# Optimization experiments

Measured on AMD Instinct MI355X. Metric: run time of the kernel, lower is better.

The kernel has to match this reference:

```python
import jax, jax.numpy as jnp
import numpy as np

N, E, G = 100_000, 1_200_000, 256
EPS = 1e-5

def _bn(a, g, b):
    # BatchNorm1d in training mode: biased batch statistics over dim 0
    mu = a.mean(0)
    var = ((a - mu) ** 2).mean(0)
    return (a - mu) * jax.lax.rsqrt(var + EPS) * g + b

def _cgconv(x, src, dst, ea, Wf, bf, Ws, bs, g, b):
    # PyG CGConv: z = [x_i, x_j, edge_attr]; m = sigmoid(lin_f(z)) * softplus(lin_s(z));
    # out = BN(scatter_add(m -> dst)) + x
    z = jnp.concatenate([x[dst], x[src], ea], axis=-1)      # [E, 2*64+1]
    m = jax.nn.sigmoid(z @ Wf + bf) * jax.nn.softplus(z @ Ws + bs)  # [E, 64]
    agg = jax.ops.segment_sum(m, dst, num_segments=x.shape[0])
    return _bn(agg, g, b) + x

def setup_inputs() -> dict:
    key = jax.random.key(0)
    ks = jax.random.split(key, 16)
    def w(k, shape, scale):
        return jax.random.normal(k, shape, jnp.float32) * scale
    inp = {
        "x": jax.random.normal(ks[0], (N, 12), jnp.float32),
        "edge_index": jax.random.randint(ks[1], (2, E), 0, N, jnp.int32),
        "edge_attr": jax.random.uniform(ks[2], (E, 1), dtype=jnp.float32),
        "batch": jnp.sort(jax.random.randint(ks[3], (N,), 0, G, jnp.int32)),
        "W_in": w(ks[4], (12, 64), 0.3), "b_in": jnp.zeros((64,), jnp.float32),
        "g0": jnp.ones((64,), jnp.float32), "beta0": jnp.zeros((64,), jnp.float32),
    }
    i = 5
    for l in (1, 2, 3):
        inp[f"Wf{l}"] = w(ks[i], (129, 64), 0.1)
        inp[f"bf{l}"] = jnp.zeros((64,), jnp.float32)
        inp[f"Ws{l}"] = w(ks[i + 1], (129, 64), 0.1)
        inp[f"bs{l}"] = jnp.zeros((64,), jnp.float32)
        inp[f"g{l}"] = jnp.ones((64,), jnp.float32)
        inp[f"bb{l}"] = jnp.zeros((64,), jnp.float32)
        i += 2
    inp["W1"] = w(ks[11], (64, 32), 0.15)
    inp["b1"] = jnp.zeros((32,), jnp.float32)
    inp["W2"] = w(ks[12], (32, 1), 0.2)
    inp["b2"] = jnp.zeros((1,), jnp.float32)
    return inp

def reference(x, edge_index, edge_attr, batch,
              W_in, b_in, g0, beta0,
              Wf1, bf1, Ws1, bs1, g1, bb1,
              Wf2, bf2, Ws2, bs2, g2, bb2,
              Wf3, bf3, Ws3, bs3, g3, bb3,
              W1, b1, W2, b2):
    src, dst = edge_index[0], edge_index[1]
    h = jax.nn.relu(_bn(x @ W_in + b_in, g0, beta0))
    h = jax.nn.relu(_cgconv(h, src, dst, edge_attr, Wf1, bf1, Ws1, bs1, g1, bb1))
    h = jax.nn.relu(_cgconv(h, src, dst, edge_attr, Wf2, bf2, Ws2, bs2, g2, bb2))
    h = _cgconv(h, src, dst, edge_attr, Wf3, bf3, Ws3, bs3, g3, bb3)
    # global_mean_pool
    s = jax.ops.segment_sum(h, batch, num_segments=G)
    c = jax.ops.segment_sum(jnp.ones((h.shape[0],), h.dtype), batch, num_segments=G)
    pooled = s / jnp.maximum(c, 1.0)[:, None]
    return jax.nn.relu(pooled @ W1 + b1) @ W2 + b2  # [G, 1]
```

## Files before the change

### kernel.cpp

```cpp
#include <hip/hip_runtime.h>
#include <math.h>

#define N_NODES 100000
#define N_EDGES 1200000
#define N_GRAPHS 256
#define CH 64
#define NC (N_NODES * CH)
#define EPS 1e-5f
#define LOG2E 1.4426950408889634f
#define LN2 0.6931471805599453f
#define EA_SCALE 32768.0f

#define SCAN_NB 98
#define ZSTRN 72
#define GTILES ((N_NODES + 63) / 64)
#define EA_BLOCKS 4096
#define NW (EA_BLOCKS * 4)
#define POOL_BLOCKS 256
#define WP2ROWS 64

#define NCOLORS 8
#define SC_BLOCKS 2048
#define NCHUNK (SC_BLOCKS / NCOLORS)
#define CSZ ((N_EDGES + NCHUNK - 1) / NCHUNK)
#define RNODES ((N_NODES + NCOLORS - 1) / NCOLORS)

typedef _Float16 half8 __attribute__((ext_vector_type(8)));
typedef _Float16 half2v __attribute__((ext_vector_type(2)));
typedef float floatx4 __attribute__((ext_vector_type(4)));

__device__ __forceinline__ int lbound(const int* __restrict__ a, int n, int v) {
    int lo = 0, hi = n;
    while (lo < hi) {
        int mid = (lo + hi) >> 1;
        if (a[mid] < v) lo = mid + 1; else hi = mid;
    }
    return lo;
}

__device__ __forceinline__ float gate2(float f2, float s2) {
    float ef = __builtin_amdgcn_exp2f(-f2);
    float sig = __builtin_amdgcn_rcpf(1.0f + ef);
    float es = __builtin_amdgcn_exp2f(-fabsf(s2));
    float sp = fmaxf(s2, 0.0f) + __builtin_amdgcn_logf(1.0f + es);
    return sig * sp;
}

__global__ void embed_stats_kernel(const float* __restrict__ x,
                                   const float* __restrict__ W,
                                   const float* __restrict__ b,
                                   float* __restrict__ out,
                                   float* __restrict__ stats) {
    int c = threadIdx.x & 63;
    int sub = threadIdx.x >> 6;
    float s = 0.f, q = 0.f;
    for (int r = blockIdx.x * 4 + sub; r < N_NODES; r += gridDim.x * 4) {
        const float* xr = x + r * 12;
        float acc = b[c];
#pragma unroll
        for (int k = 0; k < 12; ++k)
            acc = fmaf(xr[k], W[k * CH + c], acc);
        out[(size_t)r * CH + c] = acc;
        s += acc;
        q = fmaf(acc, acc, q);
    }
    __shared__ float ls[4][64];
    __shared__ float lq[4][64];
    ls[sub][c] = s;
    lq[sub][c] = q;
    __syncthreads();
    if (sub == 0) {
        s = ls[0][c] + ls[1][c] + ls[2][c] + ls[3][c];
        q = lq[0][c] + lq[1][c] + lq[2][c] + lq[3][c];
        atomicAdd(&stats[c], s);
        atomicAdd(&stats[64 + c], q);
    }
}

__global__ void hist_kernel(const int* __restrict__ ei,
                            int* __restrict__ rowptr) {
    const int j = blockIdx.x & (NCOLORS - 1);
    const int k = blockIdx.x >> 3;
    const int dlo = j * RNODES;
    const int dhi = min(N_NODES, dlo + RNODES);
    const int e0 = k * CSZ;
    const int e1 = min(N_EDGES, e0 + CSZ);
    for (int e = e0 + threadIdx.x; e < e1; e += 256) {
        int d = ei[N_EDGES + e];
        if (d >= dlo && d < dhi) atomicAdd(&rowptr[d + 1], 1);
    }
}

__global__ void scanA_kernel(int* __restrict__ a, int* __restrict__ btot) {
    __shared__ int wsum[16];
    int t = threadIdx.x, lane = t & 63, w = t >> 6;
    int i = blockIdx.x * 1024 + t;
    int v = (i <= N_NODES) ? a[i] : 0;
    int s = v;
#pragma unroll
    for (int d = 1; d < 64; d <<= 1) {
        int o = __shfl_up(s, d);
        if (lane >= d) s += o;
    }
    if (lane == 63) wsum[w] = s;
    __syncthreads();
    if (w == 0) {
        int ws2 = (lane < 16) ? wsum[lane] : 0;
#pragma unroll
        for (int d = 1; d < 16; d <<= 1) {
            int o = __shfl_up(ws2, d);
            if (lane >= d) ws2 += o;
        }
        if (lane < 16) wsum[lane] = ws2;
    }
    __syncthreads();
    int off = (w > 0) ? wsum[w - 1] : 0;
    if (i <= N_NODES) a[i] = s + off;
    if (t == 0) btot[blockIdx.x] = wsum[15];
}

__global__ void scanB_kernel(int* __restrict__ btot) {
    int lane = threadIdx.x;
    int carry = 0;
    for (int base = 0; base < SCAN_NB; base += 64) {
        int i = base + lane;
        int v = (i < SCAN_NB) ? btot[i] : 0;
        int s = v;
#pragma unroll
        for (int d = 1; d < 64; d <<= 1) {
            int o = __shfl_up(s, d);
            if (lane >= d) s += o;
        }
        if (i < SCAN_NB) btot[i] = s + carry;
        carry += __shfl(s, 63);
    }
}

__global__ void scanC_kernel(int* __restrict__ a, const int* __restrict__ btot,
                             int* __restrict__ cursor) {
    int i = blockIdx.x * 1024 + threadIdx.x;
    int off = (blockIdx.x > 0) ? btot[blockIdx.x - 1] : 0;
    if (i <= N_NODES) {
        int val = a[i] + off;
        a[i] = val;
        if (i < N_NODES) cursor[i] = val;
    }
}

__global__ void scatter_kernel(const int* __restrict__ ei,
                               const float* __restrict__ ea,
                               int* __restrict__ cursor,
                               unsigned* __restrict__ sef,
                               const int* __restrict__ rowptr,
                               int* __restrict__ wrange) {
    int gid = blockIdx.x * blockDim.x + threadIdx.x;
    if (gid <= NW) {
        if (gid == NW) wrange[NW] = N_NODES;
        else {
            int e0t = (int)((long)gid * N_EDGES / NW);
            wrange[gid] = lbound(rowptr, N_NODES + 1, e0t);
        }
    }
    if (gid < 8) sef[N_EDGES + gid] = 0u;
    const int j = blockIdx.x & (NCOLORS - 1);
    const int k = blockIdx.x >> 3;
    const int dlo = j * RNODES;
    const int dhi = min(N_NODES, dlo + RNODES);
    const int e0 = k * CSZ;
    const int e1 = min(N_EDGES, e0 + CSZ);
    for (int e = e0 + threadIdx.x; e < e1; e += 256) {
        int d = ei[N_EDGES + e];
        if (d >= dlo && d < dhi) {
            int pos = atomicAdd(&cursor[d], 1);
            unsigned v = ((unsigned)ei[e] << 15) | (unsigned)(ea[e] * EA_SCALE);
            sef[pos] = v;
        }
    }
}

__global__ void prep_weights_kernel(const float* __restrict__ Wf0, const float* __restrict__ Ws0,
                                    const float* __restrict__ bf0, const float* __restrict__ bs0,
                                    const float* __restrict__ Wf1, const float* __restrict__ Ws1,
                                    const float* __restrict__ bf1, const float* __restrict__ bs1,
                                    const float* __restrict__ Wf2, const float* __restrict__ Ws2,
                                    const float* __restrict__ bf2, const float* __restrict__ bs2,
                                    _Float16* __restrict__ WT2,
                                    float* __restrict__ w128,
                                    float* __restrict__ bias) {
    int gid = blockIdx.x * blockDim.x + threadIdx.x;
    int l = gid >> 14;
    int idx = gid & 16383;
    if (l >= 3) return;
    const float* Wf = (l == 0) ? Wf0 : (l == 1) ? Wf1 : Wf2;
    const float* Ws = (l == 0) ? Ws0 : (l == 1) ? Ws1 : Ws2;
    const float* bf = (l == 0) ? bf0 : (l == 1) ? bf1 : bf2;
    const float* bs = (l == 0) ? bs0 : (l == 1) ? bs1 : bs2;
    {
        int cc = idx >> 6;
        int k = idx & 63;
        float v;
        if (cc < 128) {
            int ch = cc >> 1;
            v = (cc & 1) ? Ws[k * 64 + ch] : Wf[k * 64 + ch];
        } else {
            int j = cc - 128, ch = j >> 1;
            v = (j & 1) ? Ws[(64 + k) * 64 + ch] : Wf[(64 + k) * 64 + ch];
        }
        WT2[l * 16384 + idx] = (_Float16)(v * LOG2E);
    }
    if (idx < 128) {
        w128[l * 128 + idx] = ((idx < 64) ? Wf[128 * 64 + idx] : Ws[128 * 64 + (idx - 64)])
                              * (LOG2E / EA_SCALE);
        bias[l * 128 + idx] = ((idx < 64) ? bf[idx] : bs[idx - 64]) * LOG2E;
    }
}

template <bool RES, bool RED, bool A16>
__global__ __launch_bounds__(256)
void node_gemm_kernel(const void* __restrict__ ain,
                      const float* __restrict__ res,
                      const float* __restrict__ stats,
                      const float* __restrict__ gamma,
                      const float* __restrict__ beta,
                      const _Float16* __restrict__ WT2,
                      float* __restrict__ hout,
                      _Float16* __restrict__ pqrs) {
    __shared__ __align__(16) _Float16 As[64 * ZSTRN];
    __shared__ __align__(16) float ab[128];
    __shared__ float sw[128];
    const int t = threadIdx.x;
    const int lane = t & 63;
    const int w = t >> 6;
    const int l15 = lane & 15;
    const int quad = lane >> 4;

    if (RED) {
        if (t < 128) {
            float s = 0.f;
#pragma unroll 8
            for (int r = 0; r < WP2ROWS; ++r) s += stats[r * 128 + t];
            sw[t] = s;
        }
        __syncthreads();
    }
    if (t < 64) {
        float s0 = RED ? sw[t] : stats[t];
        float s1 = RED ? sw[64 + t] : stats[64 + t];
        float mean = s0 * (1.0f / (float)N_NODES);
        float var  = s1 * (1.0f / (float)N_NODES) - mean * mean;
        float inv  = rsqrtf(var + EPS);
        float A = gamma[t] * inv;
        ab[t] = A;
        ab[64 + t] = beta[t] - mean * A;
    }

    half8 bfr[4][2];
#pragma unroll
    for (int tt = 0; tt < 4; ++tt)
#pragma unroll
        for (int ks = 0; ks < 2; ++ks)
            bfr[tt][ks] = *(const half8*)(WT2 + (w * 64 + tt * 16 + l15) * 64 + ks * 32 + quad * 8);
    __syncthreads();

    const int base = blockIdx.x * 64;
    {
        const int e = t >> 2, q = t & 3;
        const int row = base + e;
        const bool valid = (row < N_NODES);
        const int crow = valid ? row : (N_NODES - 1);
        const float* rp = res + (size_t)crow * CH + q * 16;
        float af[16];
        if (A16) {
            const _Float16* aph = (const _Float16*)ain + (size_t)crow * CH + q * 16;
            half8 h0 = *(const half8*)aph;
            half8 h1 = *(const half8*)(aph + 8);
#pragma unroll
            for (int j = 0; j < 8; ++j) { af[j] = (float)h0[j]; af[8 + j] = (float)h1[j]; }
        } else {
            const float* ap = (const float*)ain + (size_t)crow * CH + q * 16;
#pragma unroll
            for (int i = 0; i < 4; ++i) {
                float4 a4 = *(const float4*)(ap + i * 4);
                af[i * 4 + 0] = a4.x; af[i * 4 + 1] = a4.y;
                af[i * 4 + 2] = a4.z; af[i * 4 + 3] = a4.w;
            }
        }
        float vv[16];
#pragma unroll
        for (int i = 0; i < 4; ++i) {
            float4 A4 = *(const float4*)(ab + q * 16 + i * 4);
            float4 B4 = *(const float4*)(ab + 64 + q * 16 + i * 4);
            float rx = 0.f, ry = 0.f, rz = 0.f, rw = 0.f;
            if (RES) {
                float4 r4 = *(const float4*)(rp + i * 4);
                rx = r4.x; ry = r4.y; rz = r4.z; rw = r4.w;
            }
            vv[i * 4 + 0] = fmaxf(fmaf(af[i * 4 + 0], A4.x, B4.x) + rx, 0.0f);
            vv[i * 4 + 1] = fmaxf(fmaf(af[i * 4 + 1], A4.y, B4.y) + ry, 0.0f);
            vv[i * 4 + 2] = fmaxf(fmaf(af[i * 4 + 2], A4.z, B4.z) + rz, 0.0f);
            vv[i * 4 + 3] = fmaxf(fmaf(af[i * 4 + 3], A4.w, B4.w) + rw, 0.0f);
        }
        if (valid) {
            float* hp = hout + (size_t)row * CH + q * 16;
#pragma unroll
            for (int i = 0; i < 4; ++i)
                *(float4*)(hp + i * 4) = make_float4(vv[i * 4], vv[i * 4 + 1], vv[i * 4 + 2], vv[i * 4 + 3]);
        }
        half8 o;
#pragma unroll
        for (int j = 0; j < 8; ++j) o[j] = (_Float16)vv[j];
        *(half8*)(As + e * ZSTRN + q * 16) = o;
#pragma unroll
        for (int j = 0; j < 8; ++j) o[j] = (_Float16)vv[8 + j];
        *(half8*)(As + e * ZSTRN + q * 16 + 8) = o;
    }
    __syncthreads();

    floatx4 acc[4][4];
#pragma unroll
    for (int rt = 0; rt < 4; ++rt)
#pragma unroll
        for (int tt = 0; tt < 4; ++tt)
#pragma unroll
            for (int r = 0; r < 4; ++r) acc[rt][tt][r] = 0.f;

#pragma unroll
    for (int ks = 0; ks < 2; ++ks) {
#pragma unroll
        for (int rt = 0; rt < 4; ++rt) {
            half8 a = *(const half8*)(As + (rt * 16 + l15) * ZSTRN + ks * 32 + quad * 8);
#pragma unroll
            for (int tt = 0; tt < 4; ++tt)
                acc[rt][tt] = __builtin_amdgcn_mfma_f32_16x16x32_f16(a, bfr[tt][ks], acc[rt][tt], 0, 0, 0);
        }
    }

#pragma unroll
    for (int rt = 0; rt < 4; ++rt) {
#pragma unroll
        for (int r = 0; r < 4; ++r) {
            int row = base + rt * 16 + quad * 4 + r;
            if (row < N_NODES) {
#pragma unroll
                for (int tt = 0; tt < 4; ++tt)
                    pqrs[(size_t)row * 256 + w * 64 + tt * 16 + l15] = (_Float16)acc[rt][tt][r];
            }
        }
    }
}

__global__ __launch_bounds__(256)
void edge_agg_kernel(const _Float16* __restrict__ pqrs,
                     const unsigned* __restrict__ sef,
                     const int* __restrict__ rowptr,
                     const int* __restrict__ wrange,
                     const float* __restrict__ w128,
                     const float* __restrict__ bias,
                     _Float16* __restrict__ agg,
                     float* __restrict__ wpart2) {
    const int lane = threadIdx.x & 63;
    const int w = threadIdx.x >> 6;
    const int gw = __builtin_amdgcn_readfirstlane(blockIdx.x * 4 + w);
    const float wfc = w128[lane], wsc = w128[64 + lane];
    const float bfc = bias[lane], bsc = bias[64 + lane];
    const half2v* __restrict__ prb = (const half2v*)pqrs;
    const half2v* __restrict__ qsb = (const half2v*)pqrs + 64;

    const int n0 = wrange[gw];
    const int n1 = wrange[gw + 1];

    float ssum = 0.f, sqsum = 0.f;
    for (int n = n0; n < n1; ++n) {
        const int rs = rowptr[n], re = rowptr[n + 1];
        half2v pr = prb[(size_t)n * 128 + lane];
        const float fb = (float)pr[0] + bfc;
        const float sb = (float)pr[1] + bsc;
        float acc0 = 0.f, acc1 = 0.f, acc2 = 0.f, acc3 = 0.f;
        int e = rs;
        for (; e + 8 <= re; e += 8) {
            unsigned s0 = sef[e],     s1 = sef[e + 1], s2 = sef[e + 2], s3 = sef[e + 3];
            unsigned s4 = sef[e + 4], s5 = sef[e + 5], s6 = sef[e + 6], s7 = sef[e + 7];
            half2v q0 = qsb[(size_t)(s0 >> 15) * 128 + lane];
            half2v q1 = qsb[(size_t)(s1 >> 15) * 128 + lane];
            half2v q2 = qsb[(size_t)(s2 >> 15) * 128 + lane];
            half2v q3 = qsb[(size_t)(s3 >> 15) * 128 + lane];
            half2v q4 = qsb[(size_t)(s4 >> 15) * 128 + lane];
            half2v q5 = qsb[(size_t)(s5 >> 15) * 128 + lane];
            half2v q6 = qsb[(size_t)(s6 >> 15) * 128 + lane];
            half2v q7 = qsb[(size_t)(s7 >> 15) * 128 + lane];
            float ea0 = (float)(s0 & 32767u), ea1 = (float)(s1 & 32767u);
            float ea2 = (float)(s2 & 32767u), ea3 = (float)(s3 & 32767u);
            float ea4 = (float)(s4 & 32767u), ea5 = (float)(s5 & 32767u);
            float ea6 = (float)(s6 & 32767u), ea7 = (float)(s7 & 32767u);
            acc0 += gate2(fmaf(ea0, wfc, fb + (float)q0[0]), fmaf(ea0, wsc, sb + (float)q0[1]));
            acc1 += gate2(fmaf(ea1, wfc, fb + (float)q1[0]), fmaf(ea1, wsc, sb + (float)q1[1]));
            acc2 += gate2(fmaf(ea2, wfc, fb + (float)q2[0]), fmaf(ea2, wsc, sb + (float)q2[1]));
            acc3 += gate2(fmaf(ea3, wfc, fb + (float)q3[0]), fmaf(ea3, wsc, sb + (float)q3[1]));
            acc0 += gate2(fmaf(ea4, wfc, fb + (float)q4[0]), fmaf(ea4, wsc, sb + (float)q4[1]));
            acc1 += gate2(fmaf(ea5, wfc, fb + (float)q5[0]), fmaf(ea5, wsc, sb + (float)q5[1]));
            acc2 += gate2(fmaf(ea6, wfc, fb + (float)q6[0]), fmaf(ea6, wsc, sb + (float)q6[1]));
            acc3 += gate2(fmaf(ea7, wfc, fb + (float)q7[0]), fmaf(ea7, wsc, sb + (float)q7[1]));
        }
        if (e + 4 <= re) {
            unsigned s0 = sef[e], s1 = sef[e + 1], s2 = sef[e + 2], s3 = sef[e + 3];
            half2v q0 = qsb[(size_t)(s0 >> 15) * 128 + lane];
            half2v q1 = qsb[(size_t)(s1 >> 15) * 128 + lane];
            half2v q2 = qsb[(size_t)(s2 >> 15) * 128 + lane];
            half2v q3 = qsb[(size_t)(s3 >> 15) * 128 + lane];
            float ea0 = (float)(s0 & 32767u), ea1 = (float)(s1 & 32767u);
            float ea2 = (float)(s2 & 32767u), ea3 = (float)(s3 & 32767u);
            acc0 += gate2(fmaf(ea0, wfc, fb + (float)q0[0]), fmaf(ea0, wsc, sb + (float)q0[1]));
            acc1 += gate2(fmaf(ea1, wfc, fb + (float)q1[0]), fmaf(ea1, wsc, sb + (float)q1[1]));
            acc2 += gate2(fmaf(ea2, wfc, fb + (float)q2[0]), fmaf(ea2, wsc, sb + (float)q2[1]));
            acc3 += gate2(fmaf(ea3, wfc, fb + (float)q3[0]), fmaf(ea3, wsc, sb + (float)q3[1]));
            e += 4;
        }
        for (; e < re; ++e) {
            unsigned s0 = sef[e];
            half2v q0 = qsb[(size_t)(s0 >> 15) * 128 + lane];
            float ea0 = (float)(s0 & 32767u);
            acc0 += gate2(fmaf(ea0, wfc, fb + (float)q0[0]), fmaf(ea0, wsc, sb + (float)q0[1]));
        }
        _Float16 ah = (_Float16)(LN2 * ((acc0 + acc1) + (acc2 + acc3)));
        agg[(size_t)n * CH + lane] = ah;
        float acc = (float)ah;
        ssum += acc;
        sqsum = fmaf(acc, acc, sqsum);
    }
    __shared__ float reds[4][128];
    reds[w][lane] = ssum;
    reds[w][64 + lane] = sqsum;
    __syncthreads();
    if (w == 0) {
        float a = reds[0][lane] + reds[1][lane] + reds[2][lane] + reds[3][lane];
        float b = reds[0][64 + lane] + reds[1][64 + lane] + reds[2][64 + lane] + reds[3][64 + lane];
        float* wp = wpart2 + (size_t)(blockIdx.x & (WP2ROWS - 1)) * 128;
        atomicAdd(&wp[lane], a);
        atomicAdd(&wp[64 + lane], b);
    }
}

__global__ __launch_bounds__(256)
void pool_bn_kernel(const _Float16* __restrict__ ain,
                    const float* __restrict__ res,
                    const float* __restrict__ wp2,
                    const float* __restrict__ gamma,
                    const float* __restrict__ beta,
                    const int* __restrict__ batch,
                    float* __restrict__ pooled,
                    float* __restrict__ counts) {
    __shared__ float sw[128];
    __shared__ float ab[128];
    if (threadIdx.x < 128) {
        float s = 0.f;
#pragma unroll 8
        for (int r = 0; r < WP2ROWS; ++r) s += wp2[r * 128 + threadIdx.x];
        sw[threadIdx.x] = s;
    }
    __syncthreads();
    if (threadIdx.x < 64) {
        int t = threadIdx.x;
        float mean = sw[t] * (1.0f / (float)N_NODES);
        float var  = sw[64 + t] * (1.0f / (float)N_NODES) - mean * mean;
        float inv  = rsqrtf(var + EPS);
        float A = gamma[t] * inv;
        ab[t] = A;
        ab[64 + t] = beta[t] - mean * A;
    }
    __syncthreads();

    const int c = threadIdx.x & 63;
    const float A = ab[c], B = ab[64 + c];
    const int walker = blockIdx.x * 4 + (threadIdx.x >> 6);
    const int nwalk = POOL_BLOCKS * 4;
    const int chunk = (N_NODES + nwalk - 1) / nwalk;
    int r0 = walker * chunk;
    int r1 = min(N_NODES, r0 + chunk);
    if (r0 >= r1) return;

    int cur = batch[r0];
    float acc = 0.0f;
    int runlen = 0;
    for (int r = r0; r < r1; ++r) {
        int b = batch[r];
        if (b != cur) {
            atomicAdd(&pooled[cur * CH + c], acc);
            if (c == 0) atomicAdd(&counts[cur], (float)runlen);
            acc = 0.0f;
            runlen = 0;
            cur = b;
        }
        size_t idx = (size_t)r * CH + c;
        acc += fmaf((float)ain[idx], A, B) + res[idx];
        ++runlen;
    }
    atomicAdd(&pooled[cur * CH + c], acc);
    if (c == 0) atomicAdd(&counts[cur], (float)runlen);
}

__global__ void head_kernel(const float* __restrict__ pooled,
                            const float* __restrict__ counts,
                            const float* __restrict__ W1,
                            const float* __restrict__ b1,
                            const float* __restrict__ W2,
                            const float* __restrict__ b2,
                            float* __restrict__ out) {
    int gph = blockIdx.x;
    int t = threadIdx.x;
    __shared__ float p[64];
    __shared__ float h1[32];
    float cnt = fmaxf(counts[gph], 1.0f);
    p[t] = pooled[gph * CH + t] / cnt;
    __syncthreads();
    if (t < 32) {
        float acc = b1[t];
#pragma unroll
        for (int c = 0; c < 64; ++c)
            acc = fmaf(p[c], W1[c * 32 + t], acc);
        h1[t] = fmaxf(acc, 0.0f);
    }
    __syncthreads();
    if (t == 0) {
        float acc = b2[0];
#pragma unroll
        for (int j = 0; j < 32; ++j)
            acc = fmaf(h1[j], W2[j], acc);
        out[gph] = acc;
    }
}

extern "C" void kernel_launch(void* const* d_in, const int* in_sizes, int n_in,
                              void* d_out, int out_size, void* d_ws, size_t ws_size,
                              hipStream_t stream) {
    const float* x     = (const float*)d_in[0];
    const int*   ei    = (const int*)d_in[1];
    const float* ea    = (const float*)d_in[2];
    const int*   batch = (const int*)d_in[3];
    const float* W_in  = (const float*)d_in[4];
    const float* b_in  = (const float*)d_in[5];
    const float* g0    = (const float*)d_in[6];
    const float* beta0 = (const float*)d_in[7];

    const float* Wf[3] = {(const float*)d_in[8],  (const float*)d_in[14], (const float*)d_in[20]};
    const float* bfv[3]= {(const float*)d_in[9],  (const float*)d_in[15], (const float*)d_in[21]};
    const float* Wsv[3]= {(const float*)d_in[10], (const float*)d_in[16], (const float*)d_in[22]};
    const float* bsv[3]= {(const float*)d_in[11], (const float*)d_in[17], (const float*)d_in[23]};
    const float* gm[3] = {(const float*)d_in[12], (const float*)d_in[18], (const float*)d_in[24]};
    const float* bb[3] = {(const float*)d_in[13], (const float*)d_in[19], (const float*)d_in[25]};

    const float* W1 = (const float*)d_in[26];
    const float* b1 = (const float*)d_in[27];
    const float* W2 = (const float*)d_in[28];
    const float* b2 = (const float*)d_in[29];

    float* out = (float*)d_out;

#define ALIGN256(v) (((v) + 255) & ~(size_t)255)
    char* base = (char*)d_ws;
    size_t off = 0;
    float* bufA = (float*)(base + off);       off = ALIGN256(off + (size_t)NC * 4);
    float* bufB = (float*)(base + off);       off = ALIGN256(off + (size_t)NC * 4);
    _Float16* AGG = (_Float16*)(base + off);  off = ALIGN256(off + (size_t)NC * 2);
    _Float16* WT2 = (_Float16*)(base + off);  off = ALIGN256(off + 3 * 256 * 64 * 2);
    float* w128   = (float*)(base + off);     off = ALIGN256(off + 3 * 128 * 4);
    float* biasL  = (float*)(base + off);     off = ALIGN256(off + 3 * 128 * 4);
    int* cursor   = (int*)(base + off);       off = ALIGN256(off + (size_t)N_NODES * 4);
    unsigned* sef = (unsigned*)(base + off);  off = ALIGN256(off + (size_t)(N_EDGES + 8) * 4);
    _Float16* pqrs = (_Float16*)(base + off); off = ALIGN256(off + (size_t)N_NODES * 256 * 2);
    int* wrange   = (int*)(base + off);       off = ALIGN256(off + (size_t)(NW + 1) * 4);
    char* zbase   = base + off;
    int* rowptr   = (int*)(base + off);       off = ALIGN256(off + (size_t)(N_NODES + 1) * 4);
    int* btot     = (int*)(base + off);       off = ALIGN256(off + SCAN_NB * 4);
    float* stats0 = (float*)(base + off);     off = ALIGN256(off + 128 * 4);
    float* wpart2 = (float*)(base + off);     off = ALIGN256(off + 3 * WP2ROWS * 128 * 4);
    float* pooled = (float*)(base + off);     off = ALIGN256(off + (size_t)N_GRAPHS * CH * 4);
    float* counts = (float*)(base + off);     off = ALIGN256(off + (size_t)N_GRAPHS * 4);
    size_t zbytes = (size_t)(base + off - zbase);

    hipMemsetAsync(zbase, 0, zbytes, stream);

    hist_kernel<<<SC_BLOCKS, 256, 0, stream>>>(ei, rowptr);
    scanA_kernel<<<SCAN_NB, 1024, 0, stream>>>(rowptr, btot);
    scanB_kernel<<<1, 64, 0, stream>>>(btot);
    scanC_kernel<<<SCAN_NB, 1024, 0, stream>>>(rowptr, btot, cursor);
    scatter_kernel<<<SC_BLOCKS, 256, 0, stream>>>(ei, ea, cursor, sef, rowptr, wrange);

    prep_weights_kernel<<<192, 256, 0, stream>>>(
        Wf[0], Wsv[0], bfv[0], bsv[0],
        Wf[1], Wsv[1], bfv[1], bsv[1],
        Wf[2], Wsv[2], bfv[2], bsv[2],
        WT2, w128, biasL);

    embed_stats_kernel<<<512, 256, 0, stream>>>(x, W_in, b_in, bufA, stats0);

    node_gemm_kernel<false, false, false><<<GTILES, 256, 0, stream>>>(
        bufA, nullptr, stats0, g0, beta0, WT2 + 0 * 256 * 64, bufB, pqrs);
    edge_agg_kernel<<<EA_BLOCKS, 256, 0, stream>>>(
        pqrs, sef, rowptr, wrange, w128 + 0 * 128, biasL + 0 * 128, AGG,
        wpart2 + 0 * WP2ROWS * 128);

    node_gemm_kernel<true, true, true><<<GTILES, 256, 0, stream>>>(
        AGG, bufB, wpart2 + 0 * WP2ROWS * 128, gm[0], bb[0], WT2 + 1 * 256 * 64, bufA, pqrs);
    edge_agg_kernel<<<EA_BLOCKS, 256, 0, stream>>>(
        pqrs, sef, rowptr, wrange, w128 + 1 * 128, biasL + 1 * 128, AGG,
        wpart2 + 1 * WP2ROWS * 128);

    node_gemm_kernel<true, true, true><<<GTILES, 256, 0, stream>>>(
        AGG, bufA, wpart2 + 1 * WP2ROWS * 128, gm[1], bb[1], WT2 + 2 * 256 * 64, bufB, pqrs);
    edge_agg_kernel<<<EA_BLOCKS, 256, 0, stream>>>(
        pqrs, sef, rowptr, wrange, w128 + 2 * 128, biasL + 2 * 128, AGG,
        wpart2 + 2 * WP2ROWS * 128);

    pool_bn_kernel<<<POOL_BLOCKS, 256, 0, stream>>>(
        AGG, bufB, wpart2 + 2 * WP2ROWS * 128, gm[2], bb[2], batch, pooled, counts);
    head_kernel<<<N_GRAPHS, 64, 0, stream>>>(pooled, counts, W1, b1, W2, b2, out);
}
```

Before: 570.0 us.

## Store node activations in fp16, merge preprocessing kernels, prefetch node rows

```diff
diff --git a/kernel.cpp b/kernel.cpp
--- a/kernel.cpp
+++ b/kernel.cpp
@@ -25,6 +25,10 @@
 #define CSZ ((N_EDGES + NCHUNK - 1) / NCHUNK)
 #define RNODES ((N_NODES + NCOLORS - 1) / NCOLORS)
 
+#define EMB_BLOCKS 512
+#define PREP_BLOCKS 192
+#define PRE_BLOCKS (SC_BLOCKS + EMB_BLOCKS + PREP_BLOCKS)
+
 typedef _Float16 half8 __attribute__((ext_vector_type(8)));
 typedef _Float16 half2v __attribute__((ext_vector_type(2)));
 typedef float floatx4 __attribute__((ext_vector_type(4)));
@@ -46,48 +50,89 @@
     return sig * sp;
 }
 
-__global__ void embed_stats_kernel(const float* __restrict__ x,
-                                   const float* __restrict__ W,
-                                   const float* __restrict__ b,
-                                   float* __restrict__ out,
-                                   float* __restrict__ stats) {
-    int c = threadIdx.x & 63;
-    int sub = threadIdx.x >> 6;
-    float s = 0.f, q = 0.f;
-    for (int r = blockIdx.x * 4 + sub; r < N_NODES; r += gridDim.x * 4) {
-        const float* xr = x + r * 12;
-        float acc = b[c];
-#pragma unroll
-        for (int k = 0; k < 12; ++k)
-            acc = fmaf(xr[k], W[k * CH + c], acc);
-        out[(size_t)r * CH + c] = acc;
-        s += acc;
-        q = fmaf(acc, acc, q);
-    }
-    __shared__ float ls[4][64];
-    __shared__ float lq[4][64];
-    ls[sub][c] = s;
-    lq[sub][c] = q;
-    __syncthreads();
-    if (sub == 0) {
-        s = ls[0][c] + ls[1][c] + ls[2][c] + ls[3][c];
-        q = lq[0][c] + lq[1][c] + lq[2][c] + lq[3][c];
-        atomicAdd(&stats[c], s);
-        atomicAdd(&stats[64 + c], q);
-    }
-}
-
-__global__ void hist_kernel(const int* __restrict__ ei,
-                            int* __restrict__ rowptr) {
-    const int j = blockIdx.x & (NCOLORS - 1);
-    const int k = blockIdx.x >> 3;
-    const int dlo = j * RNODES;
-    const int dhi = min(N_NODES, dlo + RNODES);
-    const int e0 = k * CSZ;
-    const int e1 = min(N_EDGES, e0 + CSZ);
-    for (int e = e0 + threadIdx.x; e < e1; e += 256) {
-        int d = ei[N_EDGES + e];
-        if (d >= dlo && d < dhi) atomicAdd(&rowptr[d + 1], 1);
+__global__ void pre_kernel(const int* __restrict__ ei,
+                           int* __restrict__ rowptr,
+                           const float* __restrict__ x,
+                           const float* __restrict__ W,
+                           const float* __restrict__ b,
+                           _Float16* __restrict__ emb,
+                           float* __restrict__ stats,
+                           const float* __restrict__ Wf0, const float* __restrict__ Ws0,
+                           const float* __restrict__ bf0, const float* __restrict__ bs0,
+                           const float* __restrict__ Wf1, const float* __restrict__ Ws1,
+                           const float* __restrict__ bf1, const float* __restrict__ bs1,
+                           const float* __restrict__ Wf2, const float* __restrict__ Ws2,
+                           const float* __restrict__ bf2, const float* __restrict__ bs2,
+                           _Float16* __restrict__ WT2,
+                           float* __restrict__ w128,
+                           float* __restrict__ bias) {
+    const int bid = blockIdx.x;
+    if (bid < SC_BLOCKS) {
+        const int j = bid & (NCOLORS - 1);
+        const int k = bid >> 3;
+        const int dlo = j * RNODES;
+        const int dhi = min(N_NODES, dlo + RNODES);
+        const int e0 = k * CSZ;
+        const int e1 = min(N_EDGES, e0 + CSZ);
+        for (int e = e0 + threadIdx.x; e < e1; e += 256) {
+            int d = ei[N_EDGES + e];
+            if (d >= dlo && d < dhi) atomicAdd(&rowptr[d + 1], 1);
+        }
+    } else if (bid < SC_BLOCKS + EMB_BLOCKS) {
+        const int eb = bid - SC_BLOCKS;
+        int c = threadIdx.x & 63;
+        int sub = threadIdx.x >> 6;
+        float s = 0.f, q = 0.f;
+        for (int r = eb * 4 + sub; r < N_NODES; r += EMB_BLOCKS * 4) {
+            const float* xr = x + r * 12;
+            float acc = b[c];
+#pragma unroll
+            for (int k = 0; k < 12; ++k)
+                acc = fmaf(xr[k], W[k * CH + c], acc);
+            _Float16 h = (_Float16)acc;
+            emb[(size_t)r * CH + c] = h;
+            float hf = (float)h;
+            s += hf;
+            q = fmaf(hf, hf, q);
+        }
+        __shared__ float ls[4][64];
+        __shared__ float lq[4][64];
+        ls[sub][c] = s;
+        lq[sub][c] = q;
+        __syncthreads();
+        if (sub == 0) {
+            s = ls[0][c] + ls[1][c] + ls[2][c] + ls[3][c];
+            q = lq[0][c] + lq[1][c] + lq[2][c] + lq[3][c];
+            atomicAdd(&stats[c], s);
+            atomicAdd(&stats[64 + c], q);
+        }
+    } else {
+        int gid = (bid - SC_BLOCKS - EMB_BLOCKS) * 256 + threadIdx.x;
+        int l = gid >> 14;
+        int idx = gid & 16383;
+        if (l >= 3) return;
+        const float* Wf = (l == 0) ? Wf0 : (l == 1) ? Wf1 : Wf2;
+        const float* Ws = (l == 0) ? Ws0 : (l == 1) ? Ws1 : Ws2;
+        const float* bf = (l == 0) ? bf0 : (l == 1) ? bf1 : bf2;
+        const float* bs = (l == 0) ? bs0 : (l == 1) ? bs1 : bs2;
+        {
+            int cc = idx >> 6;
+            int k = idx & 63;
+            float v;
+            if (cc < 128) {
+                int ch = cc >> 1;
+                v = (cc & 1) ? Ws[k * 64 + ch] : Wf[k * 64 + ch];
+            } else {
+                int jj = cc - 128, ch = jj >> 1;
+                v = (jj & 1) ? Ws[(64 + k) * 64 + ch] : Wf[(64 + k) * 64 + ch];
+            }
+            WT2[l * 16384 + idx] = (_Float16)(v * LOG2E);
+        }
+        if (idx < 128) {
+            w128[l * 128 + idx] = ((idx < 64) ? Wf[128 * 64 + idx] : Ws[128 * 64 + (idx - 64)])
+                                  * (LOG2E / EA_SCALE);
+            bias[l * 128 + idx] = ((idx < 64) ? bf[idx] : bs[idx - 64]) * LOG2E;
+        }
     }
 }
 
@@ -178,52 +223,15 @@
     }
 }
 
-__global__ void prep_weights_kernel(const float* __restrict__ Wf0, const float* __restrict__ Ws0,
-                                    const float* __restrict__ bf0, const float* __restrict__ bs0,
-                                    const float* __restrict__ Wf1, const float* __restrict__ Ws1,
-                                    const float* __restrict__ bf1, const float* __restrict__ bs1,
-                                    const float* __restrict__ Wf2, const float* __restrict__ Ws2,
-                                    const float* __restrict__ bf2, const float* __restrict__ bs2,
-                                    _Float16* __restrict__ WT2,
-                                    float* __restrict__ w128,
-                                    float* __restrict__ bias) {
-    int gid = blockIdx.x * blockDim.x + threadIdx.x;
-    int l = gid >> 14;
-    int idx = gid & 16383;
-    if (l >= 3) return;
-    const float* Wf = (l == 0) ? Wf0 : (l == 1) ? Wf1 : Wf2;
-    const float* Ws = (l == 0) ? Ws0 : (l == 1) ? Ws1 : Ws2;
-    const float* bf = (l == 0) ? bf0 : (l == 1) ? bf1 : bf2;
-    const float* bs = (l == 0) ? bs0 : (l == 1) ? bs1 : bs2;
-    {
-        int cc = idx >> 6;
-        int k = idx & 63;
-        float v;
-        if (cc < 128) {
-            int ch = cc >> 1;
-            v = (cc & 1) ? Ws[k * 64 + ch] : Wf[k * 64 + ch];
-        } else {
-            int j = cc - 128, ch = j >> 1;
-            v = (j & 1) ? Ws[(64 + k) * 64 + ch] : Wf[(64 + k) * 64 + ch];
-        }
-        WT2[l * 16384 + idx] = (_Float16)(v * LOG2E);
-    }
-    if (idx < 128) {
-        w128[l * 128 + idx] = ((idx < 64) ? Wf[128 * 64 + idx] : Ws[128 * 64 + (idx - 64)])
-                              * (LOG2E / EA_SCALE);
-        bias[l * 128 + idx] = ((idx < 64) ? bf[idx] : bs[idx - 64]) * LOG2E;
-    }
-}
-
-template <bool RES, bool RED, bool A16>
+template <bool RES, bool RED>
 __global__ __launch_bounds__(256)
-void node_gemm_kernel(const void* __restrict__ ain,
-                      const float* __restrict__ res,
+void node_gemm_kernel(const _Float16* __restrict__ ain,
+                      const _Float16* __restrict__ res,
                       const float* __restrict__ stats,
                       const float* __restrict__ gamma,
                       const float* __restrict__ beta,
                       const _Float16* __restrict__ WT2,
-                      float* __restrict__ hout,
+                      _Float16* __restrict__ hout,
                       _Float16* __restrict__ pqrs) {
     __shared__ __align__(16) _Float16 As[64 * ZSTRN];
     __shared__ __align__(16) float ab[128];
@@ -268,51 +276,45 @@
         const int row = base + e;
         const bool valid = (row < N_NODES);
         const int crow = valid ? row : (N_NODES - 1);
-        const float* rp = res + (size_t)crow * CH + q * 16;
         float af[16];
-        if (A16) {
-            const _Float16* aph = (const _Float16*)ain + (size_t)crow * CH + q * 16;
+        {
+            const _Float16* aph = ain + (size_t)crow * CH + q * 16;
             half8 h0 = *(const half8*)aph;
             half8 h1 = *(const half8*)(aph + 8);
 #pragma unroll
             for (int j = 0; j < 8; ++j) { af[j] = (float)h0[j]; af[8 + j] = (float)h1[j]; }
-        } else {
-            const float* ap = (const float*)ain + (size_t)crow * CH + q * 16;
-#pragma unroll
-            for (int i = 0; i < 4; ++i) {
-                float4 a4 = *(const float4*)(ap + i * 4);
-                af[i * 4 + 0] = a4.x; af[i * 4 + 1] = a4.y;
-                af[i * 4 + 2] = a4.z; af[i * 4 + 3] = a4.w;
-            }
+        }
+        float rf[16];
+        if (RES) {
+            const _Float16* rph = res + (size_t)crow * CH + q * 16;
+            half8 r0 = *(const half8*)rph;
+            half8 r1 = *(const half8*)(rph + 8);
+#pragma unroll
+            for (int j = 0; j < 8; ++j) { rf[j] = (float)r0[j]; rf[8 + j] = (float)r1[j]; }
         }
         float vv[16];
 #pragma unroll
         for (int i = 0; i < 4; ++i) {
             float4 A4 = *(const float4*)(ab + q * 16 + i * 4);
             float4 B4 = *(const float4*)(ab + 64 + q * 16 + i * 4);
-            float rx = 0.f, ry = 0.f, rz = 0.f, rw = 0.f;
-            if (RES) {
-                float4 r4 = *(const float4*)(rp + i * 4);
-                rx = r4.x; ry = r4.y; rz = r4.z; rw = r4.w;
+#pragma unroll
+            for (int jj = 0; jj < 4; ++jj) {
+                float Ax = (jj == 0) ? A4.x : (jj == 1) ? A4.y : (jj == 2) ? A4.z : A4.w;
+                float Bx = (jj == 0) ? B4.x : (jj == 1) ? B4.y : (jj == 2) ? B4.z : B4.w;
+                float r = RES ? rf[i * 4 + jj] : 0.f;
+                vv[i * 4 + jj] = fmaxf(fmaf(af[i * 4 + jj], Ax, Bx) + r, 0.0f);
             }
-            vv[i * 4 + 0] = fmaxf(fmaf(af[i * 4 + 0], A4.x, B4.x) + rx, 0.0f);
-            vv[i * 4 + 1] = fmaxf(fmaf(af[i * 4 + 1], A4.y, B4.y) + ry, 0.0f);
-            vv[i * 4 + 2] = fmaxf(fmaf(af[i * 4 + 2], A4.z, B4.z) + rz, 0.0f);
-            vv[i * 4 + 3] = fmaxf(fmaf(af[i * 4 + 3], A4.w, B4.w) + rw, 0.0f);
-        }
+        }
+        half8 o0, o1;
+#pragma unroll
+        for (int j = 0; j < 8; ++j) { o0[j] = (_Float16)vv[j]; o1[j] = (_Float16)vv[8 + j]; }
+        *(half8*)(As + e * ZSTRN + q * 16) = o0;
+        *(half8*)(As + e * ZSTRN + q * 16 + 8) = o1;
         if (valid) {
-            float* hp = hout + (size_t)row * CH + q * 16;
-#pragma unroll
-            for (int i = 0; i < 4; ++i)
-                *(float4*)(hp + i * 4) = make_float4(vv[i * 4], vv[i * 4 + 1], vv[i * 4 + 2], vv[i * 4 + 3]);
-        }
-        half8 o;
-#pragma unroll
-        for (int j = 0; j < 8; ++j) o[j] = (_Float16)vv[j];
-        *(half8*)(As + e * ZSTRN + q * 16) = o;
-#pragma unroll
-        for (int j = 0; j < 8; ++j) o[j] = (_Float16)vv[8 + j];
-        *(half8*)(As + e * ZSTRN + q * 16 + 8) = o;
+            half8* hp = (half8*)(hout + (size_t)row * CH + q * 16);
+            hp[0] = o0;
+            hp[1] = o1;
+        }
     }
     __syncthreads();
 
@@ -370,62 +372,69 @@
     const int n1 = wrange[gw + 1];
 
     float ssum = 0.f, sqsum = 0.f;
-    for (int n = n0; n < n1; ++n) {
-        const int rs = rowptr[n], re = rowptr[n + 1];
-        half2v pr = prb[(size_t)n * 128 + lane];
-        const float fb = (float)pr[0] + bfc;
-        const float sb = (float)pr[1] + bsc;
-        float acc0 = 0.f, acc1 = 0.f, acc2 = 0.f, acc3 = 0.f;
-        int e = rs;
-        for (; e + 8 <= re; e += 8) {
-            unsigned s0 = sef[e],     s1 = sef[e + 1], s2 = sef[e + 2], s3 = sef[e + 3];
-            unsigned s4 = sef[e + 4], s5 = sef[e + 5], s6 = sef[e + 6], s7 = sef[e + 7];
-            half2v q0 = qsb[(size_t)(s0 >> 15) * 128 + lane];
-            half2v q1 = qsb[(size_t)(s1 >> 15) * 128 + lane];
-            half2v q2 = qsb[(size_t)(s2 >> 15) * 128 + lane];
-            half2v q3 = qsb[(size_t)(s3 >> 15) * 128 + lane];
-            half2v q4 = qsb[(size_t)(s4 >> 15) * 128 + lane];
-            half2v q5 = qsb[(size_t)(s5 >> 15) * 128 + lane];
-            half2v q6 = qsb[(size_t)(s6 >> 15) * 128 + lane];
-            half2v q7 = qsb[(size_t)(s7 >> 15) * 128 + lane];
-            float ea0 = (float)(s0 & 32767u), ea1 = (float)(s1 & 32767u);
-            float ea2 = (float)(s2 & 32767u), ea3 = (float)(s3 & 32767u);
-            float ea4 = (float)(s4 & 32767u), ea5 = (float)(s5 & 32767u);
-            float ea6 = (float)(s6 & 32767u), ea7 = (float)(s7 & 32767u);
-            acc0 += gate2(fmaf(ea0, wfc, fb + (float)q0[0]), fmaf(ea0, wsc, sb + (float)q0[1]));
-            acc1 += gate2(fmaf(ea1, wfc, fb + (float)q1[0]), fmaf(ea1, wsc, sb + (float)q1[1]));
-            acc2 += gate2(fmaf(ea2, wfc, fb + (float)q2[0]), fmaf(ea2, wsc, sb + (float)q2[1]));
-            acc3 += gate2(fmaf(ea3, wfc, fb + (float)q3[0]), fmaf(ea3, wsc, sb + (float)q3[1]));
-            acc0 += gate2(fmaf(ea4, wfc, fb + (float)q4[0]), fmaf(ea4, wsc, sb + (float)q4[1]));
-            acc1 += gate2(fmaf(ea5, wfc, fb + (float)q5[0]), fmaf(ea5, wsc, sb + (float)q5[1]));
-            acc2 += gate2(fmaf(ea6, wfc, fb + (float)q6[0]), fmaf(ea6, wsc, sb + (float)q6[1]));
-            acc3 += gate2(fmaf(ea7, wfc, fb + (float)q7[0]), fmaf(ea7, wsc, sb + (float)q7[1]));
-        }
-        if (e + 4 <= re) {
-            unsigned s0 = sef[e], s1 = sef[e + 1], s2 = sef[e + 2], s3 = sef[e + 3];
-            half2v q0 = qsb[(size_t)(s0 >> 15) * 128 + lane];
-            half2v q1 = qsb[(size_t)(s1 >> 15) * 128 + lane];
-            half2v q2 = qsb[(size_t)(s2 >> 15) * 128 + lane];
-            half2v q3 = qsb[(size_t)(s3 >> 15) * 128 + lane];
-            float ea0 = (float)(s0 & 32767u), ea1 = (float)(s1 & 32767u);
-            float ea2 = (float)(s2 & 32767u), ea3 = (float)(s3 & 32767u);
-            acc0 += gate2(fmaf(ea0, wfc, fb + (float)q0[0]), fmaf(ea0, wsc, sb + (float)q0[1]));
-            acc1 += gate2(fmaf(ea1, wfc, fb + (float)q1[0]), fmaf(ea1, wsc, sb + (float)q1[1]));
-            acc2 += gate2(fmaf(ea2, wfc, fb + (float)q2[0]), fmaf(ea2, wsc, sb + (float)q2[1]));
-            acc3 += gate2(fmaf(ea3, wfc, fb + (float)q3[0]), fmaf(ea3, wsc, sb + (float)q3[1]));
-            e += 4;
-        }
-        for (; e < re; ++e) {
-            unsigned s0 = sef[e];
-            half2v q0 = qsb[(size_t)(s0 >> 15) * 128 + lane];
-            float ea0 = (float)(s0 & 32767u);
-            acc0 += gate2(fmaf(ea0, wfc, fb + (float)q0[0]), fmaf(ea0, wsc, sb + (float)q0[1]));
-        }
-        _Float16 ah = (_Float16)(LN2 * ((acc0 + acc1) + (acc2 + acc3)));
-        agg[(size_t)n * CH + lane] = ah;
-        float acc = (float)ah;
-        ssum += acc;
-        sqsum = fmaf(acc, acc, sqsum);
+    if (n0 < n1) {
+        half2v prn = prb[(size_t)n0 * 128 + lane];
+        for (int n = n0; n < n1; ++n) {
+            const int rs = rowptr[n], re = rowptr[n + 1];
+            half2v pr = prn;
+            {
+                int np = (n + 1 < N_NODES) ? (n + 1) : (N_NODES - 1);
+                prn = prb[(size_t)np * 128 + lane];
+            }
+            const float fb = (float)pr[0] + bfc;
+            const float sb = (float)pr[1] + bsc;
+            float acc0 = 0.f, acc1 = 0.f, acc2 = 0.f, acc3 = 0.f;
+            int e = rs;
+            for (; e + 8 <= re; e += 8) {
+                unsigned s0 = sef[e],     s1 = sef[e + 1], s2 = sef[e + 2], s3 = sef[e + 3];
+                unsigned s4 = sef[e + 4], s5 = sef[e + 5], s6 = sef[e + 6], s7 = sef[e + 7];
+                half2v q0 = qsb[(size_t)(s0 >> 15) * 128 + lane];
+                half2v q1 = qsb[(size_t)(s1 >> 15) * 128 + lane];
+                half2v q2 = qsb[(size_t)(s2 >> 15) * 128 + lane];
+                half2v q3 = qsb[(size_t)(s3 >> 15) * 128 + lane];
+                half2v q4 = qsb[(size_t)(s4 >> 15) * 128 + lane];
+                half2v q5 = qsb[(size_t)(s5 >> 15) * 128 + lane];
+                half2v q6 = qsb[(size_t)(s6 >> 15) * 128 + lane];
+                half2v q7 = qsb[(size_t)(s7 >> 15) * 128 + lane];
+                float ea0 = (float)(s0 & 32767u), ea1 = (float)(s1 & 32767u);
+                float ea2 = (float)(s2 & 32767u), ea3 = (float)(s3 & 32767u);
+                float ea4 = (float)(s4 & 32767u), ea5 = (float)(s5 & 32767u);
+                float ea6 = (float)(s6 & 32767u), ea7 = (float)(s7 & 32767u);
+                acc0 += gate2(fmaf(ea0, wfc, fb + (float)q0[0]), fmaf(ea0, wsc, sb + (float)q0[1]));
+                acc1 += gate2(fmaf(ea1, wfc, fb + (float)q1[0]), fmaf(ea1, wsc, sb + (float)q1[1]));
+                acc2 += gate2(fmaf(ea2, wfc, fb + (float)q2[0]), fmaf(ea2, wsc, sb + (float)q2[1]));
+                acc3 += gate2(fmaf(ea3, wfc, fb + (float)q3[0]), fmaf(ea3, wsc, sb + (float)q3[1]));
+                acc0 += gate2(fmaf(ea4, wfc, fb + (float)q4[0]), fmaf(ea4, wsc, sb + (float)q4[1]));
+                acc1 += gate2(fmaf(ea5, wfc, fb + (float)q5[0]), fmaf(ea5, wsc, sb + (float)q5[1]));
+                acc2 += gate2(fmaf(ea6, wfc, fb + (float)q6[0]), fmaf(ea6, wsc, sb + (float)q6[1]));
+                acc3 += gate2(fmaf(ea7, wfc, fb + (float)q7[0]), fmaf(ea7, wsc, sb + (float)q7[1]));
+            }
+            if (e + 4 <= re) {
+                unsigned s0 = sef[e], s1 = sef[e + 1], s2 = sef[e + 2], s3 = sef[e + 3];
+                half2v q0 = qsb[(size_t)(s0 >> 15) * 128 + lane];
+                half2v q1 = qsb[(size_t)(s1 >> 15) * 128 + lane];
+                half2v q2 = qsb[(size_t)(s2 >> 15) * 128 + lane];
+                half2v q3 = qsb[(size_t)(s3 >> 15) * 128 + lane];
+                float ea0 = (float)(s0 & 32767u), ea1 = (float)(s1 & 32767u);
+                float ea2 = (float)(s2 & 32767u), ea3 = (float)(s3 & 32767u);
+                acc0 += gate2(fmaf(ea0, wfc, fb + (float)q0[0]), fmaf(ea0, wsc, sb + (float)q0[1]));
+                acc1 += gate2(fmaf(ea1, wfc, fb + (float)q1[0]), fmaf(ea1, wsc, sb + (float)q1[1]));
+                acc2 += gate2(fmaf(ea2, wfc, fb + (float)q2[0]), fmaf(ea2, wsc, sb + (float)q2[1]));
+                acc3 += gate2(fmaf(ea3, wfc, fb + (float)q3[0]), fmaf(ea3, wsc, sb + (float)q3[1]));
+                e += 4;
+            }
+            for (; e < re; ++e) {
+                unsigned s0 = sef[e];
+                half2v q0 = qsb[(size_t)(s0 >> 15) * 128 + lane];
+                float ea0 = (float)(s0 & 32767u);
+                acc0 += gate2(fmaf(ea0, wfc, fb + (float)q0[0]), fmaf(ea0, wsc, sb + (float)q0[1]));
+            }
+            _Float16 ah = (_Float16)(LN2 * ((acc0 + acc1) + (acc2 + acc3)));
+            agg[(size_t)n * CH + lane] = ah;
+            float acc = (float)ah;
+            ssum += acc;
+            sqsum = fmaf(acc, acc, sqsum);
+        }
     }
     __shared__ float reds[4][128];
     reds[w][lane] = ssum;
@@ -442,7 +451,7 @@
 
 __global__ __launch_bounds__(256)
 void pool_bn_kernel(const _Float16* __restrict__ ain,
-                    const float* __restrict__ res,
+                    const _Float16* __restrict__ res,
                     const float* __restrict__ wp2,
                     const float* __restrict__ gamma,
                     const float* __restrict__ beta,
@@ -491,7 +500,7 @@
             cur = b;
         }
         size_t idx = (size_t)r * CH + c;
-        acc += fmaf((float)ain[idx], A, B) + res[idx];
+        acc += fmaf((float)ain[idx], A, B) + (float)res[idx];
         ++runlen;
     }
     atomicAdd(&pooled[cur * CH + c], acc);
@@ -558,8 +567,8 @@
 #define ALIGN256(v) (((v) + 255) & ~(size_t)255)
     char* base = (char*)d_ws;
     size_t off = 0;
-    float* bufA = (float*)(base + off);       off = ALIGN256(off + (size_t)NC * 4);
-    float* bufB = (float*)(base + off);       off = ALIGN256(off + (size_t)NC * 4);
+    _Float16* bufA = (_Float16*)(base + off); off = ALIGN256(off + (size_t)NC * 2);
+    _Float16* bufB = (_Float16*)(base + off); off = ALIGN256(off + (size_t)NC * 2);
     _Float16* AGG = (_Float16*)(base + off);  off = ALIGN256(off + (size_t)NC * 2);
     _Float16* WT2 = (_Float16*)(base + off);  off = ALIGN256(off + 3 * 256 * 64 * 2);
     float* w128   = (float*)(base + off);     off = ALIGN256(off + 3 * 128 * 4);
@@ -579,33 +588,31 @@
 
     hipMemsetAsync(zbase, 0, zbytes, stream);
 
-    hist_kernel<<<SC_BLOCKS, 256, 0, stream>>>(ei, rowptr);
+    pre_kernel<<<PRE_BLOCKS, 256, 0, stream>>>(
+        ei, rowptr, x, W_in, b_in, bufA, stats0,
+        Wf[0], Wsv[0], bfv[0], bsv[0],
+        Wf[1], Wsv[1], bfv[1], bsv[1],
+        Wf[2], Wsv[2], bfv[2], bsv[2],
+        WT2, w128, biasL);
+
     scanA_kernel<<<SCAN_NB, 1024, 0, stream>>>(rowptr, btot);
     scanB_kernel<<<1, 64, 0, stream>>>(btot);
     scanC_kernel<<<SCAN_NB, 1024, 0, stream>>>(rowptr, btot, cursor);
     scatter_kernel<<<SC_BLOCKS, 256, 0, stream>>>(ei, ea, cursor, sef, rowptr, wrange);
 
-    prep_weights_kernel<<<192, 256, 0, stream>>>(
-        Wf[0], Wsv[0], bfv[0], bsv[0],
-        Wf[1], Wsv[1], bfv[1], bsv[1],
-        Wf[2], Wsv[2], bfv[2], bsv[2],
-        WT2, w128, biasL);
-
-    embed_stats_kernel<<<512, 256, 0, stream>>>(x, W_in, b_in, bufA, stats0);
-
-    node_gemm_kernel<false, false, false><<<GTILES, 256, 0, stream>>>(
+    node_gemm_kernel<false, false><<<GTILES, 256, 0, stream>>>(
         bufA, nullptr, stats0, g0, beta0, WT2 + 0 * 256 * 64, bufB, pqrs);
     edge_agg_kernel<<<EA_BLOCKS, 256, 0, stream>>>(
         pqrs, sef, rowptr, wrange, w128 + 0 * 128, biasL + 0 * 128, AGG,
         wpart2 + 0 * WP2ROWS * 128);
 
-    node_gemm_kernel<true, true, true><<<GTILES, 256, 0, stream>>>(
+    node_gemm_kernel<true, true><<<GTILES, 256, 0, stream>>>(
         AGG, bufB, wpart2 + 0 * WP2ROWS * 128, gm[0], bb[0], WT2 + 1 * 256 * 64, bufA, pqrs);
     edge_agg_kernel<<<EA_BLOCKS, 256, 0, stream>>>(
         pqrs, sef, rowptr, wrange, w128 + 1 * 128, biasL + 1 * 128, AGG,
         wpart2 + 1 * WP2ROWS * 128);
 
-    node_gemm_kernel<true, true, true><<<GTILES, 256, 0, stream>>>(
+    node_gemm_kernel<true, true><<<GTILES, 256, 0, stream>>>(
         AGG, bufA, wpart2 + 1 * WP2ROWS * 128, gm[1], bb[1], WT2 + 2 * 256 * 64, bufB, pqrs);
     edge_agg_kernel<<<EA_BLOCKS, 256, 0, stream>>>(
         pqrs, sef, rowptr, wrange, w128 + 2 * 128, biasL + 2 * 128, AGG,
```

Result: faster. 550.8 us (-3.4%).
